# Kernel optimization log

Measured on AMD Instinct MI355X. Metric: run time of the kernel, lower is better.

Reference implementation:

```python
import jax, jax.numpy as jnp
import numpy as np

N_LEVELS = 16
F = 2
LOG2_T = 19
T = 1 << LOG2_T
BASE_RES = 16.0
FINEST_RES = 512.0
N_SAMPLES = 128
NEAR, FAR = 2.0, 6.0
BOX_MIN = jnp.array([-1.5, -1.5, -1.5], jnp.float32)
BOX_MAX = jnp.array([1.5, 1.5, 1.5], jnp.float32)
GEO_FEAT = 15
OUT_CH = 4

_PRIMES = np.array([1, 2654435761, 805459861], dtype=np.uint32)
_OFFSETS = np.array([[i, j, k] for i in (0, 1) for j in (0, 1) for k in (0, 1)], dtype=np.int32)  # [8,3]
_B = np.exp((np.log(FINEST_RES) - np.log(BASE_RES)) / (N_LEVELS - 1))
_RESOLUTIONS = np.floor(BASE_RES * _B ** np.arange(N_LEVELS)).astype(np.float32)


def setup_inputs() -> dict:
    key = jax.random.key(0)
    ks = jax.random.split(key, 10)
    n_rays = 16384
    o = jax.random.uniform(ks[0], (n_rays, 3), jnp.float32, -0.5, 0.5)
    d = jax.random.normal(ks[1], (n_rays, 3), jnp.float32)
    d = d / jnp.linalg.norm(d, axis=-1, keepdims=True)
    rays = jnp.concatenate([o, d], -1)
    hash_tables = jax.random.uniform(ks[2], (N_LEVELS, T, F), jnp.float32, -1e-4, 1e-4)
    def w(k, di, do):
        return jax.random.normal(k, (di, do), jnp.float32) * (1.0 / np.sqrt(di))
    return dict(
        rays=rays,
        hash_tables=hash_tables,
        ws0=w(ks[3], 32, 64), ws1=w(ks[4], 64, 64), ws2=w(ks[5], 64, 1 + GEO_FEAT),
        wc0=w(ks[6], 16 + GEO_FEAT, 64), wc1=w(ks[7], 64, 64), wc2=w(ks[8], 64, 64), wc3=w(ks[9], 64, OUT_CH - 1),
    )


def _hash_embed(x, tables):
    """Multi-res hash grid: x [P,3] world coords, tables [L,T,F] -> ([P,L*F], keep_mask [P])."""
    xc = jnp.clip(x, BOX_MIN, BOX_MAX)
    keep = jnp.all(x == xc, axis=-1)
    offs = jnp.asarray(_OFFSETS)          # [8,3]
    primes = jnp.asarray(_PRIMES)         # uint32
    feats = []
    for l in range(N_LEVELS):
        grid = (BOX_MAX - BOX_MIN) / _RESOLUTIONS[l]
        bl = jnp.floor((xc - BOX_MIN) / grid).astype(jnp.int32)   # [P,3] bottom-left voxel index
        vmin = bl.astype(jnp.float32) * grid + BOX_MIN
        wts = (xc - vmin) / grid                                  # trilinear weights [P,3]
        corners = (bl[:, None, :] + offs[None]).astype(jnp.uint32)  # [P,8,3]
        h = (corners[..., 0] * primes[0]) ^ (corners[..., 1] * primes[1]) ^ (corners[..., 2] * primes[2])
        idx = (h & jnp.uint32(T - 1)).astype(jnp.int32)           # [P,8]
        e = tables[l][idx]                                        # [P,8,F]
        w0, w1, w2 = wts[:, 0:1], wts[:, 1:2], wts[:, 2:3]
        c00 = e[:, 0] * (1 - w0) + e[:, 4] * w0
        c01 = e[:, 1] * (1 - w0) + e[:, 5] * w0
        c10 = e[:, 2] * (1 - w0) + e[:, 6] * w0
        c11 = e[:, 3] * (1 - w0) + e[:, 7] * w0
        c0 = c00 * (1 - w1) + c10 * w1
        c1 = c01 * (1 - w1) + c11 * w1
        feats.append(c0 * (1 - w2) + c1 * w2)
    return jnp.concatenate(feats, -1), keep


def _sh_encode(d):
    """Degree-4 spherical harmonics encoding, [P,3] -> [P,16]."""
    x, y, z = d[..., 0], d[..., 1], d[..., 2]
    xx, yy, zz = x * x, y * y, z * z
    xy, yz, xz = x * y, y * z, x * z
    C0 = 0.28209479177387814
    C1 = 0.4886025119029199
    C2 = (1.0925484305920792, -1.0925484305920792, 0.31539156525252005, -1.0925484305920792, 0.5462742152960396)
    C3 = (-0.5900435899266435, 2.890611442640554, -0.4570457994644658, 0.3731763325901154,
          -0.4570457994644658, 1.445305721320277, -0.5900435899266435)
    return jnp.stack([
        jnp.full_like(x, C0),
        -C1 * y, C1 * z, -C1 * x,
        C2[0] * xy, C2[1] * yz, C2[2] * (2.0 * zz - xx - yy), C2[3] * xz, C2[4] * (xx - yy),
        C3[0] * y * (3.0 * xx - yy), C3[1] * xy * z, C3[2] * y * (4.0 * zz - xx - yy),
        C3[3] * z * (2.0 * zz - 3.0 * xx - 3.0 * yy), C3[4] * x * (4.0 * zz - xx - yy),
        C3[5] * z * (xx - yy), C3[6] * x * (xx - 3.0 * yy),
    ], axis=-1)


def _forward(rays, hash_tables, ws0, ws1, ws2, wc0, wc1, wc2, wc3):
    n_rays = rays.shape[0]
    o, d = rays[:, :3], rays[:, 3:6]
    z = jnp.linspace(NEAR, FAR, N_SAMPLES, dtype=jnp.float32)
    zvals = jnp.broadcast_to(z, (n_rays, N_SAMPLES))
    pts = o[:, None, :] + d[:, None, :] * z[None, :, None]       # [N,S,3]
    P = n_rays * N_SAMPLES
    pts_f = pts.reshape(P, 3)
    dirs_f = jnp.broadcast_to(d[:, None, :], (n_rays, N_SAMPLES, 3)).reshape(P, 3)

    enc_pts, keep = _hash_embed(pts_f, hash_tables)              # [P,32], [P]
    enc_dirs = _sh_encode(dirs_f)                                # [P,16]

    # NeRFSmall: bias-free sigma net then color net
    h = jnp.maximum(enc_pts @ ws0, 0.0)
    h = jnp.maximum(h @ ws1, 0.0)
    h = h @ ws2                                                   # [P, 1+GEO_FEAT]
    sigma, geo = h[:, 0], h[:, 1:]
    hc = jnp.concatenate([enc_dirs, geo], -1)
    hc = jnp.maximum(hc @ wc0, 0.0)
    hc = jnp.maximum(hc @ wc1, 0.0)
    hc = jnp.maximum(hc @ wc2, 0.0)
    color = hc @ wc3                                              # [P, OUT_CH-1]

    sigma = jnp.where(keep, sigma, 0.0)                           # output[~keep_mask, -1] = 0
    raw = jnp.concatenate([color, sigma[:, None]], -1).reshape(n_rays, N_SAMPLES, OUT_CH)

    # Integrator (raw2outputs)
    dists = zvals[:, 1:] - zvals[:, :-1]
    dists = jnp.concatenate([dists, jnp.full((n_rays, 1), 1e10, jnp.float32)], -1)
    dists = dists * jnp.linalg.norm(d, axis=-1, keepdims=True)
    chs = jax.nn.sigmoid(raw[..., :-1])
    alpha = 1.0 - jnp.exp(-jnp.maximum(raw[..., -1], 0.0) * dists)
    trans = jnp.cumprod(1.0 - alpha + 1e-10, axis=-1)
    trans = jnp.concatenate([jnp.ones((n_rays, 1), jnp.float32), trans[:, :-1]], -1)
    weights = alpha * trans
    chs_map = jnp.einsum('ns,nsc->nc', weights, chs)
    depth_map = jnp.sum(weights * zvals, -1)
    probs = jnp.concatenate([weights, 1.0 - jnp.sum(weights, -1, keepdims=True) + 1e-6], -1)
    p = probs / jnp.sum(probs, -1, keepdims=True)
    sparsity_loss = -jnp.sum(p * jnp.log(jnp.clip(p, 1e-37)), -1)
    return chs_map, depth_map, sparsity_loss


def reference(rays, hash_tables, ws0, ws1, ws2, wc0, wc1, wc2, wc3):
    return _forward(rays, hash_tables, ws0, ws1, ws2, wc0, wc1, wc2, wc3)
```

## Files before the change

### kernel.cpp

```cpp
#include <hip/hip_runtime.h>

#define NRAYS 16384
#define NLEV  16
#define THASH 524288
#define MAXACT 48
#define MAXPTS (NRAYS*MAXACT)
#define MBLK  512
#define MGRID 1024

__device__ __forceinline__ float zval32(int i) {
  const float step = 4.0f / 127.0f;
  return __fadd_rn(2.0f, __fmul_rn((float)i, step));
}
__device__ __forceinline__ float pcoord(float o, float d, float z) {
  return __fadd_rn(o, __fmul_rn(d, z));
}

__global__ __launch_bounds__(64)
void k_classify(const float* __restrict__ rays,
                float* __restrict__ sh,
                unsigned* __restrict__ counter,
                unsigned* __restrict__ rbase,
                unsigned* __restrict__ rn,
                unsigned* __restrict__ plist) {
  int r = blockIdx.x * 64 + threadIdx.x;
  if (r >= NRAYS) return;
  float ox = rays[6*r+0], oy = rays[6*r+1], oz = rays[6*r+2];
  float dx = rays[6*r+3], dy = rays[6*r+4], dz = rays[6*r+5];
  float x = dx, y = dy, z = dz;
  float xx = x*x, yy = y*y, zz = z*z, xy = x*y, yz = y*z, xz = x*z;
  float* shp = sh + 16*r;
  shp[0]  = 0.28209479177387814f;
  shp[1]  = -0.4886025119029199f * y;
  shp[2]  =  0.4886025119029199f * z;
  shp[3]  = -0.4886025119029199f * x;
  shp[4]  =  1.0925484305920792f * xy;
  shp[5]  = -1.0925484305920792f * yz;
  shp[6]  =  0.31539156525252005f * (2.0f*zz - xx - yy);
  shp[7]  = -1.0925484305920792f * xz;
  shp[8]  =  0.5462742152960396f * (xx - yy);
  shp[9]  = -0.5900435899266435f * y * (3.0f*xx - yy);
  shp[10] =  2.890611442640554f  * xy * z;
  shp[11] = -0.4570457994644658f * y * (4.0f*zz - xx - yy);
  shp[12] =  0.3731763325901154f * z * (2.0f*zz - 3.0f*xx - 3.0f*yy);
  shp[13] = -0.4570457994644658f * x * (4.0f*zz - xx - yy);
  shp[14] =  1.445305721320277f  * z * (xx - yy);
  shp[15] = -0.5900435899266435f * x * (xx - 3.0f*yy);
  int n = 0;
  for (int i = 0; i < 128; ++i) {
    float zi = zval32(i);
    float px = pcoord(ox, dx, zi);
    float py = pcoord(oy, dy, zi);
    float pz = pcoord(oz, dz, zi);
    bool in = (px >= -1.5f) && (px <= 1.5f) && (py >= -1.5f) && (py <= 1.5f)
           && (pz >= -1.5f) && (pz <= 1.5f);
    if (!in) break;
    ++n;
  }
  unsigned base = atomicAdd(counter, (unsigned)n);
  rbase[r] = base;
  rn[r]    = (unsigned)n;
  for (int i = 0; i < n; ++i) plist[base + i] = (unsigned)(r*128 + i);
}

template<int IN, int TOTOUT, int JC, bool RELU>
__device__ __forceinline__ void layer(const float* __restrict__ W, int jbase,
                                      const float* __restrict__ in,
                                      float* __restrict__ out, int lane) {
  float acc[JC];
#pragma unroll
  for (int j = 0; j < JC; ++j) acc[j] = 0.0f;
#pragma unroll 4
  for (int k = 0; k < IN; ++k) {
    float a = in[k*64 + lane];
    const float* Wk = W + k*TOTOUT + jbase;
#pragma unroll
    for (int j = 0; j < JC; ++j) acc[j] = fmaf(a, Wk[j], acc[j]);
  }
#pragma unroll
  for (int j = 0; j < JC; ++j)
    out[(jbase + j)*64 + lane] = RELU ? fmaxf(acc[j], 0.0f) : acc[j];
}

__global__ __launch_bounds__(MBLK)
void k_mlp(const float* __restrict__ rays,
           const float* __restrict__ tables,
           const float* __restrict__ w_s0, const float* __restrict__ w_s1,
           const float* __restrict__ w_s2, const float* __restrict__ w_c0,
           const float* __restrict__ w_c1, const float* __restrict__ w_c2,
           const float* __restrict__ w_c3,
           const float* __restrict__ sh,
           const unsigned* __restrict__ counter,
           const unsigned* __restrict__ plist,
           float4* __restrict__ results) {
  __shared__ float bufA[64*64];
  __shared__ float bufB[64*64];
  __shared__ float sig_s[64];
  __shared__ unsigned pid_s[64];
  const int t = threadIdx.x;
  const int lane = t & 63;
  const int q = __builtin_amdgcn_readfirstlane(t >> 6);
  const unsigned count = *counter;
  const unsigned ntiles = (count + 63u) >> 6;
  const float RESF[NLEV] = {16.f,20.f,25.f,32.f,40.f,50.f,64.f,80.f,
                            101.f,128.f,161.f,203.f,256.f,322.f,406.f,512.f};
  for (unsigned tile = blockIdx.x; tile < ntiles; tile += MGRID) {
    unsigned s0 = tile << 6;
    if (t < 64) {
      unsigned s = s0 + (unsigned)t;
      pid_s[t] = (s < count) ? plist[s] : 0u;
    }
    __syncthreads();
    {
      unsigned pid = pid_s[lane];
      int r = (int)(pid >> 7);
      int i = (int)(pid & 127u);
      float zi = zval32(i);
      float px = pcoord(rays[6*r+0], rays[6*r+3], zi);
      float py = pcoord(rays[6*r+1], rays[6*r+4], zi);
      float pz = pcoord(rays[6*r+2], rays[6*r+5], zi);
      float xcx = fminf(fmaxf(px, -1.5f), 1.5f);
      float xcy = fminf(fmaxf(py, -1.5f), 1.5f);
      float xcz = fminf(fmaxf(pz, -1.5f), 1.5f);
#pragma unroll
      for (int li = 0; li < 2; ++li) {
        int l = 2*q + li;
        const float grid = 3.0f / RESF[l];
        float bfx = floorf(__fdiv_rn(__fadd_rn(xcx, 1.5f), grid));
        float bfy = floorf(__fdiv_rn(__fadd_rn(xcy, 1.5f), grid));
        float bfz = floorf(__fdiv_rn(__fadd_rn(xcz, 1.5f), grid));
        float vmx = __fadd_rn(__fmul_rn(bfx, grid), -1.5f);
        float vmy = __fadd_rn(__fmul_rn(bfy, grid), -1.5f);
        float vmz = __fadd_rn(__fmul_rn(bfz, grid), -1.5f);
        float wx = __fdiv_rn(__fsub_rn(xcx, vmx), grid);
        float wy = __fdiv_rn(__fsub_rn(xcy, vmy), grid);
        float wz = __fdiv_rn(__fsub_rn(xcz, vmz), grid);
        unsigned cx0 = (unsigned)(int)bfx, cy0 = (unsigned)(int)bfy, cz0 = (unsigned)(int)bfz;
        unsigned cx1 = cx0 + 1u, cy1 = cy0 + 1u, cz1 = cz0 + 1u;
        unsigned hy0 = cy0*2654435761u, hy1 = cy1*2654435761u;
        unsigned hz0 = cz0*805459861u,  hz1 = cz1*805459861u;
        const float2* tb = (const float2*)tables + (size_t)l*THASH;
        float2 e000 = tb[(cx0^hy0^hz0)&(THASH-1)];
        float2 e001 = tb[(cx0^hy0^hz1)&(THASH-1)];
        float2 e010 = tb[(cx0^hy1^hz0)&(THASH-1)];
        float2 e011 = tb[(cx0^hy1^hz1)&(THASH-1)];
        float2 e100 = tb[(cx1^hy0^hz0)&(THASH-1)];
        float2 e101 = tb[(cx1^hy0^hz1)&(THASH-1)];
        float2 e110 = tb[(cx1^hy1^hz0)&(THASH-1)];
        float2 e111 = tb[(cx1^hy1^hz1)&(THASH-1)];
        float iwx = 1.f-wx, iwy = 1.f-wy, iwz = 1.f-wz;
        float c00a = e000.x*iwx + e100.x*wx, c00b = e000.y*iwx + e100.y*wx;
        float c01a = e001.x*iwx + e101.x*wx, c01b = e001.y*iwx + e101.y*wx;
        float c10a = e010.x*iwx + e110.x*wx, c10b = e010.y*iwx + e110.y*wx;
        float c11a = e011.x*iwx + e111.x*wx, c11b = e011.y*iwx + e111.y*wx;
        float c0a = c00a*iwy + c10a*wy, c0b = c00b*iwy + c10b*wy;
        float c1a = c01a*iwy + c11a*wy, c1b = c01b*iwy + c11b*wy;
        bufA[(2*l+0)*64 + lane] = c0a*iwz + c1a*wz;
        bufA[(2*l+1)*64 + lane] = c0b*iwz + c1b*wz;
      }
    }
    __syncthreads();
    layer<32,64,8,true >(w_s0, q*8, bufA, bufB, lane); __syncthreads();
    layer<64,64,8,true >(w_s1, q*8, bufB, bufA, lane); __syncthreads();
    layer<64,16,2,false>(w_s2, q*2, bufA, bufB, lane); __syncthreads();
    if (q == 0) sig_s[lane] = bufB[0*64 + lane];
    for (int idx = t; idx < 31*64; idx += MBLK) {
      int k = idx >> 6, p = idx & 63;
      float v;
      if (k < 16) v = sh[(pid_s[p] >> 7)*16 + k];
      else        v = bufB[(k-15)*64 + p];
      bufA[idx] = v;
    }
    __syncthreads();
    layer<31,64,8,true >(w_c0, q*8, bufA, bufB, lane); __syncthreads();
    layer<64,64,8,true >(w_c1, q*8, bufB, bufA, lane); __syncthreads();
    layer<64,64,8,true >(w_c2, q*8, bufA, bufB, lane); __syncthreads();
    if (q < 3) layer<64,3,1,false>(w_c3, q, bufB, bufA, lane);
    __syncthreads();
    if (q == 0) {
      unsigned s = s0 + (unsigned)lane;
      if (s < count) {
        float4 res;
        res.x = sig_s[lane];
        res.y = bufA[0*64 + lane];
        res.z = bufA[1*64 + lane];
        res.w = bufA[2*64 + lane];
        results[s] = res;
      }
    }
    __syncthreads();
  }
}

__global__ __launch_bounds__(64)
void k_comp(const float* __restrict__ rays,
            const unsigned* __restrict__ rbase,
            const unsigned* __restrict__ rn,
            const float4* __restrict__ results,
            float* __restrict__ out) {
  int r = blockIdx.x * 64 + threadIdx.x;
  if (r >= NRAYS) return;
  float dx = rays[6*r+3], dy = rays[6*r+4], dz = rays[6*r+5];
  float dnorm = sqrtf(dx*dx + dy*dy + dz*dz);
  int n = (int)rn[r];
  unsigned base = rbase[r];
  const float step = 4.0f/127.0f;
  const float diststep = __fmul_rn(step, dnorm);
  float S = 0.f, ch0 = 0.f, ch1 = 0.f, ch2 = 0.f, dep = 0.f, trans = 1.f;
  for (int i = 0; i < n; ++i) {
    float4 rs = results[base + i];
    float z = zval32(i);
    float sg = fmaxf(rs.x, 0.f);
    float alpha = -expm1f(-__fmul_rn(sg, diststep));
    float w = __fmul_rn(alpha, trans);
    trans = __fmul_rn(trans, __fadd_rn(__fsub_rn(1.f, alpha), 1e-10f));
    float s0 = 1.f/(1.f + expf(-rs.y));
    float s1 = 1.f/(1.f + expf(-rs.z));
    float s2 = 1.f/(1.f + expf(-rs.w));
    S += w; ch0 += w*s0; ch1 += w*s1; ch2 += w*s2; dep += w*z;
  }
  float rem  = __fadd_rn(__fsub_rn(1.f, S), 1e-6f);
  float Stot = __fadd_rn(S, rem);
  float loss = 0.f, trans2 = 1.f;
  for (int i = 0; i < n; ++i) {
    float4 rs = results[base + i];
    float sg = fmaxf(rs.x, 0.f);
    float alpha = -expm1f(-__fmul_rn(sg, diststep));
    float w = __fmul_rn(alpha, trans2);
    trans2 = __fmul_rn(trans2, __fadd_rn(__fsub_rn(1.f, alpha), 1e-10f));
    float p = __fdiv_rn(w, Stot);
    loss += p * logf(fmaxf(p, 1e-37f));
  }
  float pl = __fdiv_rn(rem, Stot);
  loss += pl * logf(fmaxf(pl, 1e-37f));
  out[3*r+0] = ch0; out[3*r+1] = ch1; out[3*r+2] = ch2;
  out[3*NRAYS + r] = dep;
  out[4*NRAYS + r] = -loss;
}

extern "C" void kernel_launch(void* const* d_in, const int* in_sizes, int n_in,
                              void* d_out, int out_size, void* d_ws, size_t ws_size,
                              hipStream_t stream) {
  const float* rays   = (const float*)d_in[0];
  const float* tables = (const float*)d_in[1];
  const float* ws0    = (const float*)d_in[2];
  const float* ws1    = (const float*)d_in[3];
  const float* ws2    = (const float*)d_in[4];
  const float* wc0    = (const float*)d_in[5];
  const float* wc1    = (const float*)d_in[6];
  const float* wc2    = (const float*)d_in[7];
  const float* wc3    = (const float*)d_in[8];

  char* ws = (char*)d_ws;
  unsigned* counter = (unsigned*)ws;
  unsigned* rbase   = (unsigned*)(ws + 256);
  unsigned* rn      = (unsigned*)(ws + 256 + 65536);
  float*    sh      = (float*)  (ws + 256 + 131072);
  float4*   results = (float4*) (ws + 1179904);
  unsigned* plist   = (unsigned*)(ws + 1179904 + (size_t)MAXPTS*16);

  hipMemsetAsync(counter, 0, 4, stream);
  k_classify<<<NRAYS/64, 64, 0, stream>>>(rays, sh, counter, rbase, rn, plist);
  k_mlp<<<MGRID, MBLK, 0, stream>>>(rays, tables, ws0, ws1, ws2,
                                    wc0, wc1, wc2, wc3, sh, counter, plist, results);
  k_comp<<<NRAYS/64, 64, 0, stream>>>(rays, rbase, rn, results, (float*)d_out);
}
```

Baseline: 186.0 us.

## Replace atomic compaction with deterministic scan and parallelize compositing per ray

Ray sample compaction moves from per-ray atomicAdd in the classify kernel to a separate single-block prefix-scan kernel. That kernel computes bases, writes the point list in ray order and sets the counter, which also removes the memset. Compositing now uses one wavefront per ray: lanes compute alpha and sigmoids in parallel into shared memory, then lane 0 runs the sequential transmittance and loss loops. This adds a kernel launch and a serial one-block scan, and relies on each ray having at most 64 samples (MAXACT 48). The ordered point list also changes the MLP's memory access pattern toward ray-contiguous locality.

```diff
diff --git a/kernel.cpp b/kernel.cpp
--- a/kernel.cpp
+++ b/kernel.cpp
@@ -19,10 +19,7 @@
 __global__ __launch_bounds__(64)
 void k_classify(const float* __restrict__ rays,
                 float* __restrict__ sh,
-                unsigned* __restrict__ counter,
-                unsigned* __restrict__ rbase,
-                unsigned* __restrict__ rn,
-                unsigned* __restrict__ plist) {
+                unsigned* __restrict__ rn) {
   int r = blockIdx.x * 64 + threadIdx.x;
   if (r >= NRAYS) return;
   float ox = rays[6*r+0], oy = rays[6*r+1], oz = rays[6*r+2];
@@ -57,10 +54,50 @@
     if (!in) break;
     ++n;
   }
-  unsigned base = atomicAdd(counter, (unsigned)n);
-  rbase[r] = base;
-  rn[r]    = (unsigned)n;
-  for (int i = 0; i < n; ++i) plist[base + i] = (unsigned)(r*128 + i);
+  rn[r] = (unsigned)n;
+}
+
+__global__ __launch_bounds__(1024)
+void k_scan(const unsigned* __restrict__ rn,
+            unsigned* __restrict__ rbase,
+            unsigned* __restrict__ counter,
+            unsigned* __restrict__ plist) {
+  __shared__ unsigned wsum[16];
+  const int t = threadIdx.x;
+  const int lane = t & 63, wid = t >> 6;
+  unsigned nv[16];
+  const uint4* rn4 = (const uint4*)rn;
+  unsigned tot = 0;
+#pragma unroll
+  for (int k = 0; k < 4; ++k) {
+    uint4 a = rn4[t*4 + k];
+    nv[4*k+0] = a.x; nv[4*k+1] = a.y; nv[4*k+2] = a.z; nv[4*k+3] = a.w;
+    tot += a.x + a.y + a.z + a.w;
+  }
+  unsigned incl = tot;
+#pragma unroll
+  for (int off = 1; off < 64; off <<= 1) {
+    unsigned v = __shfl_up(incl, off);
+    if (lane >= off) incl += v;
+  }
+  if (lane == 63) wsum[wid] = incl;
+  __syncthreads();
+  if (t == 0) {
+    unsigned acc = 0;
+#pragma unroll
+    for (int w = 0; w < 16; ++w) { unsigned x = wsum[w]; wsum[w] = acc; acc += x; }
+    *counter = acc;
+  }
+  __syncthreads();
+  unsigned base = wsum[wid] + (incl - tot);
+#pragma unroll
+  for (int j = 0; j < 16; ++j) {
+    int r = t*16 + j;
+    rbase[r] = base;
+    unsigned nj = nv[j];
+    for (unsigned i = 0; i < nj; ++i) plist[base + i] = (unsigned)(r*128) + i;
+    base += nj;
+  }
 }
 
 template<int IN, int TOTOUT, int JC, bool RELU>
@@ -192,50 +229,59 @@
   }
 }
 
-__global__ __launch_bounds__(64)
+__global__ __launch_bounds__(256)
 void k_comp(const float* __restrict__ rays,
             const unsigned* __restrict__ rbase,
             const unsigned* __restrict__ rn,
             const float4* __restrict__ results,
             float* __restrict__ out) {
-  int r = blockIdx.x * 64 + threadIdx.x;
-  if (r >= NRAYS) return;
+  __shared__ float s_al[4][64];
+  __shared__ float s_c0[4][64];
+  __shared__ float s_c1[4][64];
+  __shared__ float s_c2[4][64];
+  const int wid  = threadIdx.x >> 6;
+  const int lane = threadIdx.x & 63;
+  const int r = blockIdx.x * 4 + wid;
   float dx = rays[6*r+3], dy = rays[6*r+4], dz = rays[6*r+5];
   float dnorm = sqrtf(dx*dx + dy*dy + dz*dz);
-  int n = (int)rn[r];
-  unsigned base = rbase[r];
+  const int n = (int)rn[r];
+  const unsigned base = rbase[r];
   const float step = 4.0f/127.0f;
   const float diststep = __fmul_rn(step, dnorm);
-  float S = 0.f, ch0 = 0.f, ch1 = 0.f, ch2 = 0.f, dep = 0.f, trans = 1.f;
-  for (int i = 0; i < n; ++i) {
-    float4 rs = results[base + i];
-    float z = zval32(i);
+  if (lane < n) {
+    float4 rs = results[base + lane];
     float sg = fmaxf(rs.x, 0.f);
-    float alpha = -expm1f(-__fmul_rn(sg, diststep));
-    float w = __fmul_rn(alpha, trans);
-    trans = __fmul_rn(trans, __fadd_rn(__fsub_rn(1.f, alpha), 1e-10f));
-    float s0 = 1.f/(1.f + expf(-rs.y));
-    float s1 = 1.f/(1.f + expf(-rs.z));
-    float s2 = 1.f/(1.f + expf(-rs.w));
-    S += w; ch0 += w*s0; ch1 += w*s1; ch2 += w*s2; dep += w*z;
-  }
-  float rem  = __fadd_rn(__fsub_rn(1.f, S), 1e-6f);
-  float Stot = __fadd_rn(S, rem);
-  float loss = 0.f, trans2 = 1.f;
-  for (int i = 0; i < n; ++i) {
-    float4 rs = results[base + i];
-    float sg = fmaxf(rs.x, 0.f);
-    float alpha = -expm1f(-__fmul_rn(sg, diststep));
-    float w = __fmul_rn(alpha, trans2);
-    trans2 = __fmul_rn(trans2, __fadd_rn(__fsub_rn(1.f, alpha), 1e-10f));
-    float p = __fdiv_rn(w, Stot);
-    loss += p * logf(fmaxf(p, 1e-37f));
-  }
-  float pl = __fdiv_rn(rem, Stot);
-  loss += pl * logf(fmaxf(pl, 1e-37f));
-  out[3*r+0] = ch0; out[3*r+1] = ch1; out[3*r+2] = ch2;
-  out[3*NRAYS + r] = dep;
-  out[4*NRAYS + r] = -loss;
+    s_al[wid][lane] = -expm1f(-__fmul_rn(sg, diststep));
+    s_c0[wid][lane] = 1.f/(1.f + expf(-rs.y));
+    s_c1[wid][lane] = 1.f/(1.f + expf(-rs.z));
+    s_c2[wid][lane] = 1.f/(1.f + expf(-rs.w));
+  }
+  __syncthreads();
+  if (lane == 0) {
+    float S = 0.f, ch0 = 0.f, ch1 = 0.f, ch2 = 0.f, dep = 0.f, trans = 1.f;
+    for (int i = 0; i < n; ++i) {
+      float alpha = s_al[wid][i];
+      float w = __fmul_rn(alpha, trans);
+      trans = __fmul_rn(trans, __fadd_rn(__fsub_rn(1.f, alpha), 1e-10f));
+      S += w; ch0 += w*s_c0[wid][i]; ch1 += w*s_c1[wid][i]; ch2 += w*s_c2[wid][i];
+      dep += w*zval32(i);
+    }
+    float rem  = __fadd_rn(__fsub_rn(1.f, S), 1e-6f);
+    float Stot = __fadd_rn(S, rem);
+    float loss = 0.f, trans2 = 1.f;
+    for (int i = 0; i < n; ++i) {
+      float alpha = s_al[wid][i];
+      float w = __fmul_rn(alpha, trans2);
+      trans2 = __fmul_rn(trans2, __fadd_rn(__fsub_rn(1.f, alpha), 1e-10f));
+      float p = __fdiv_rn(w, Stot);
+      loss += p * logf(fmaxf(p, 1e-37f));
+    }
+    float pl = __fdiv_rn(rem, Stot);
+    loss += pl * logf(fmaxf(pl, 1e-37f));
+    out[3*r+0] = ch0; out[3*r+1] = ch1; out[3*r+2] = ch2;
+    out[3*NRAYS + r] = dep;
+    out[4*NRAYS + r] = -loss;
+  }
 }
 
 extern "C" void kernel_launch(void* const* d_in, const int* in_sizes, int n_in,
@@ -259,9 +305,9 @@
   float4*   results = (float4*) (ws + 1179904);
   unsigned* plist   = (unsigned*)(ws + 1179904 + (size_t)MAXPTS*16);
 
-  hipMemsetAsync(counter, 0, 4, stream);
-  k_classify<<<NRAYS/64, 64, 0, stream>>>(rays, sh, counter, rbase, rn, plist);
+  k_classify<<<NRAYS/64, 64, 0, stream>>>(rays, sh, rn);
+  k_scan<<<1, 1024, 0, stream>>>(rn, rbase, counter, plist);
   k_mlp<<<MGRID, MBLK, 0, stream>>>(rays, tables, ws0, ws1, ws2,
                                     wc0, wc1, wc2, wc3, sh, counter, plist, results);
-  k_comp<<<NRAYS/64, 64, 0, stream>>>(rays, rbase, rn, results, (float*)d_out);
-}
+  k_comp<<<NRAYS/4, 256, 0, stream>>>(rays, rbase, rn, results, (float*)d_out);
+}
```

New measurement: 206.7 us. 1.11x slower.
